# Kernel optimization log

Measured on AMD Instinct MI355X. Metric: run time of the kernel, lower is better.

Reference implementation:

```python
import jax, jax.numpy as jnp
import numpy as np

B, C, H, W = 4, 256, 64, 64
IC = C // 2  # inter_channels default = in_channels // 2


def setup_inputs() -> dict:
    key = jax.random.key(0)
    ks = jax.random.split(key, 7)
    x = jax.random.normal(ks[0], (B, C, H, W), dtype=jnp.float32)
    s = 0.02
    Wq = jax.random.normal(ks[1], (IC, C), dtype=jnp.float32) * s
    bq = jnp.zeros((IC,), dtype=jnp.float32)
    Wk = jax.random.normal(ks[2], (IC, C), dtype=jnp.float32) * s
    bk = jnp.zeros((IC,), dtype=jnp.float32)
    Wv = jax.random.normal(ks[3], (C, C), dtype=jnp.float32) * s
    bv = jnp.zeros((C,), dtype=jnp.float32)
    gamma = jnp.full((1,), 0.1, dtype=jnp.float32)  # nn.Parameter; init 0 in torch, 0.1 here for nontrivial grads
    return {"x": x, "Wq": Wq, "bq": bq, "Wk": Wk, "bk": bk, "Wv": Wv, "bv": bv, "gamma": gamma}


def reference(x, Wq, bq, Wk, bk, Wv, bv, gamma):
    b, c, h, w = x.shape
    n = h * w
    # 1x1 conv projections == per-pixel linear layers
    q = jnp.einsum('bchw,oc->bohw', x, Wq) + bq[None, :, None, None]  # [B,IC,H,W]
    k = jnp.einsum('bchw,oc->bohw', x, Wk) + bk[None, :, None, None]
    v = jnp.einsum('bchw,oc->bohw', x, Wv) + bv[None, :, None, None]  # [B,C,H,W]
    q = q.reshape(b, IC, n).transpose(0, 2, 1)  # [B,N,IC]
    k = k.reshape(b, IC, n)                     # [B,IC,N]
    v = v.reshape(b, c, n)                      # [B,C,N]
    scale = jnp.asarray(IC, x.dtype) ** -0.5
    energy = jnp.einsum('bni,bim->bnm', q, k) * scale  # [B,N,N]
    attn = jax.nn.softmax(energy, axis=-1)             # dropout is identity in eval
    # torch: out = bmm(value, attention.transpose(-1,-2)) -> out[b,c,i] = sum_j v[b,c,j]*attn[b,i,j]
    out = jnp.einsum('bcj,bij->bci', v, attn).reshape(b, c, h, w)
    return gamma[0] * out + 2.0 * x
```

## Files before the change

kernel.cpp:

```cpp
#include <hip/hip_runtime.h>
#include <stdint.h>


#define Bn 4
#define Cn 256
#define ICn 128
#define Nn 4096

typedef __attribute__((ext_vector_type(8))) short bf16x8;
typedef __attribute__((ext_vector_type(4))) float f32x4;
typedef __attribute__((ext_vector_type(16))) float f32x16;

__device__ __forceinline__ unsigned short f2bf(float f) {
  union { float f; uint32_t u; } v; v.f = f;
  uint32_t r = (v.u + 0x7fffu + ((v.u >> 16) & 1u)) >> 16;
  return (unsigned short)r;
}

__device__ __forceinline__ uint32_t pk4_fp8(float a, float b, float c, float d) {
  int r = 0;
  r = __builtin_amdgcn_cvt_pk_fp8_f32(a, b, r, false);
  r = __builtin_amdgcn_cvt_pk_fp8_f32(c, d, r, true);
  return (uint32_t)r;
}

__device__ __forceinline__ void glds16(const uint8_t* g, uint8_t* l) {
  __builtin_amdgcn_global_load_lds((const __attribute__((address_space(1))) void*)g,
                                   (__attribute__((address_space(3))) void*)l, 16, 0, 0);
}

__global__ __launch_bounds__(256) void cvt_weights(const float* __restrict__ Wq,
                                                   const float* __restrict__ Wk,
                                                   const float* __restrict__ Wv,
                                                   unsigned short* __restrict__ wbf) {
  int t = blockIdx.x * 256 + threadIdx.x;
  int tile = t >> 9;
  int kk = (t >> 6) & 7;
  int lane = t & 63;
  const float* W; int row;
  if (tile < 8)       { W = Wq; row = tile * 16 + (lane & 15); }
  else if (tile < 16) { W = Wk; row = (tile - 8) * 16 + (lane & 15); }
  else                { W = Wv; row = (tile - 16) * 16 + (lane & 15); }
  const float* src = W + (size_t)row * Cn + kk * 32 + (lane >> 4) * 8;
  float4 f0 = *(const float4*)src;
  float4 f1 = *(const float4*)(src + 4);
  ushort4 o0, o1;
  o0.x = f2bf(f0.x); o0.y = f2bf(f0.y); o0.z = f2bf(f0.z); o0.w = f2bf(f0.w);
  o1.x = f2bf(f1.x); o1.y = f2bf(f1.y); o1.z = f2bf(f1.z); o1.w = f2bf(f1.w);
  *(ushort4*)(wbf + (size_t)t * 8)     = o0;
  *(ushort4*)(wbf + (size_t)t * 8 + 4) = o1;
}

__global__ __launch_bounds__(256, 2) void proj_kernel(const float* __restrict__ x,
                                                      const unsigned short* __restrict__ wbf,
                                                      const float* __restrict__ bq,
                                                      const float* __restrict__ bk,
                                                      const float* __restrict__ bv,
                                                      uint8_t* __restrict__ qF,
                                                      uint8_t* __restrict__ kF,
                                                      uint8_t* __restrict__ vF) {
  const int b = blockIdx.y;
  const int ntile = blockIdx.x;
  const int px0 = ntile * 32;
  const int tid = threadIdx.x;
  const int lane = tid & 63;
  const int w = tid >> 6;
  const int c0 = lane & 15, g = lane >> 4;
  const float hscale = 0.2973017787506803f;

  __shared__ __align__(16) unsigned short xT[32][264];

  #pragma unroll
  for (int t = 0; t < 8; ++t) {
    int c = (tid >> 3) + t * 32;
    int i8 = tid & 7;
    float4 f4 = *(const float4*)(x + ((size_t)(b * Cn + c)) * Nn + px0 + i8 * 4);
    xT[i8 * 4 + 0][c] = f2bf(f4.x);
    xT[i8 * 4 + 1][c] = f2bf(f4.y);
    xT[i8 * 4 + 2][c] = f2bf(f4.z);
    xT[i8 * 4 + 3][c] = f2bf(f4.w);
  }
  __syncthreads();

  bf16x8 a[2][8];
  #pragma unroll
  for (int h = 0; h < 2; ++h)
    #pragma unroll
    for (int kk = 0; kk < 8; ++kk)
      a[h][kk] = *(const bf16x8*)&xT[h * 16 + c0][kk * 32 + g * 8];

  f32x4 zero = {0.f, 0.f, 0.f, 0.f};

  if (w < 2) {
    const int isq = (w == 0);
    const float* bias = isq ? bq : bk;
    uint8_t* dst = isq ? qF : kF;
    #pragma unroll
    for (int otl = 0; otl < 8; ++otl) {
      const int wt = (isq ? 0 : 8) + otl;
      bf16x8 wf[8];
      #pragma unroll
      for (int kk = 0; kk < 8; ++kk)
        wf[kk] = *(const bf16x8*)(wbf + (((size_t)wt * 8 + kk) << 9) + lane * 8);
      float4 bz = *(const float4*)(bias + otl * 16 + g * 4);
      #pragma unroll
      for (int h = 0; h < 2; ++h) {
        f32x4 acc = zero;
        #pragma unroll
        for (int kk = 0; kk < 8; ++kk)
          acc = __builtin_amdgcn_mfma_f32_16x16x32_bf16(wf[kk], a[h][kk], acc, 0, 0, 0);
        uint32_t d = pk4_fp8((acc[0] + bz.x) * hscale, (acc[1] + bz.y) * hscale,
                             (acc[2] + bz.z) * hscale, (acc[3] + bz.w) * hscale);
        size_t idx = (((((size_t)b * 128 + ntile) * 4 + (otl >> 1)) * 2 + (g >> 1)) * 32
                      + (h * 16 + c0)) * 16 + (otl & 1) * 8 + (g & 1) * 4;
        *(uint32_t*)(dst + idx) = d;
      }
    }
  } else {
    #pragma unroll
    for (int oi = 0; oi < 8; ++oi) {
      const int vtg = (w - 2) * 8 + oi;
      bf16x8 wf[8];
      #pragma unroll
      for (int kk = 0; kk < 8; ++kk)
        wf[kk] = *(const bf16x8*)(wbf + (((size_t)(16 + vtg) * 8 + kk) << 9) + lane * 8);
      const float bias = bv[vtg * 16 + c0];
      #pragma unroll
      for (int h = 0; h < 2; ++h) {
        f32x4 acc = zero;
        #pragma unroll
        for (int kk = 0; kk < 8; ++kk)
          acc = __builtin_amdgcn_mfma_f32_16x16x32_bf16(a[h][kk], wf[kk], acc, 0, 0, 0);
        uint32_t d = pk4_fp8(acc[0] + bias, acc[1] + bias, acc[2] + bias, acc[3] + bias);
        size_t idx = ((((size_t)b * 128 + ntile) * 8 + (vtg >> 1)) * 64
                      + (g >> 1) * 32 + (vtg & 1) * 16 + c0) * 16 + h * 8 + (g & 1) * 4;
        *(uint32_t*)(vF + idx) = d;
      }
    }
  }
}

__global__ __launch_bounds__(256, 2) void attn_kernel(const uint8_t* __restrict__ qF,
                                                      const uint8_t* __restrict__ kF,
                                                      const uint8_t* __restrict__ vF,
                                                      const float* __restrict__ x,
                                                      const float* __restrict__ gamma,
                                                      float* __restrict__ out) {
  const int blk = blockIdx.x;
  const int b = (blk & 7) >> 1;
  const int rg = (blk >> 3) | ((blk & 1) << 6);
  const int n0 = rg * 32;
  const int tid = threadIdx.x;
  const int L = tid & 63;
  const int ks = tid >> 6;
  const int l31 = L & 31, l5 = L >> 5;
  const bool lo = (l5 == 0);

  __shared__ __align__(16) union SM {
    uint8_t vst[4][2][8192];
    struct { float obuf[256][33]; float lsum[4][32]; } e;
  } sm;

  long qf[8];
  {
    const uint8_t* qp = qF + ((size_t)(b * 128 + rg) << 12) + L * 16;
    #pragma unroll
    for (int t = 0; t < 4; ++t) {
      union { uint4 u4; struct { uint64_t lo, hi; } s; } u;
      u.u4 = *(const uint4*)(qp + t * 1024);
      qf[2 * t] = (long)u.s.lo; qf[2 * t + 1] = (long)u.s.hi;
    }
  }

  f32x16 oacc[8];
  #pragma unroll
  for (int ct = 0; ct < 8; ++ct)
    #pragma unroll
    for (int i = 0; i < 16; ++i) oacc[ct][i] = 0.f;
  float lacc = 0.f;

  const uint8_t* kBase = kF + (((size_t)b * 128) << 12) + L * 16;
  const uint8_t* vBaseG = vF + (((size_t)b * 128) << 13);
  uint8_t* vst_w = &sm.vst[tid >> 6][0][0];

  {
    const uint8_t* vp = vBaseG + (((size_t)(ks * 32)) << 13) + (size_t)L * 16;
    #pragma unroll
    for (int ct = 0; ct < 8; ++ct)
      glds16(vp + ct * 1024, vst_w + ct * 1024);
  }
  long kfr[8];
  {
    const uint8_t* kp = kBase + (((size_t)(ks * 32)) << 12);
    #pragma unroll
    for (int t = 0; t < 4; ++t) {
      union { uint4 u4; struct { uint64_t lo, hi; } s; } u;
      u.u4 = *(const uint4*)(kp + t * 1024);
      kfr[2 * t] = (long)u.s.lo; kfr[2 * t + 1] = (long)u.s.hi;
    }
  }

  for (int it = 0; it < 32; ++it) {
    const int cur = it & 1;
    const int kb = ks * 32 + it;

    uint4 vfr[8];
    {
      const uint8_t* vl = vst_w + cur * 8192 + L * 16;
      #pragma unroll
      for (int ct = 0; ct < 8; ++ct) vfr[ct] = *(const uint4*)(vl + ct * 1024);
    }

    f32x16 s;
    #pragma unroll
    for (int i = 0; i < 16; ++i) s[i] = 0.f;
    #pragma unroll
    for (int f = 0; f < 8; ++f)
      s = __builtin_amdgcn_mfma_f32_32x32x16_fp8_fp8(kfr[f], qf[f], s, 0, 0, 0);

    if (it < 31) {
      const uint8_t* vp = vBaseG + (((size_t)(kb + 1)) << 13) + (size_t)L * 16;
      uint8_t* ldst = vst_w + (cur ^ 1) * 8192;
      #pragma unroll
      for (int ct = 0; ct < 8; ++ct)
        glds16(vp + ct * 1024, ldst + ct * 1024);
      const uint8_t* kp = kBase + (((size_t)(kb + 1)) << 12);
      #pragma unroll
      for (int t = 0; t < 4; ++t) {
        union { uint4 u4; struct { uint64_t lo, hi; } s; } u;
        u.u4 = *(const uint4*)(kp + t * 1024);
        kfr[2 * t] = (long)u.s.lo; kfr[2 * t + 1] = (long)u.s.hi;
      }
    }

    float p[16];
    #pragma unroll
    for (int i = 0; i < 16; ++i) p[i] = __expf(s[i]);
    #pragma unroll
    for (int i = 0; i < 16; ++i) lacc += p[i];
    uint32_t d0 = pk4_fp8(p[0], p[1], p[2], p[3]);
    uint32_t d1 = pk4_fp8(p[4], p[5], p[6], p[7]);
    uint32_t d2 = pk4_fp8(p[8], p[9], p[10], p[11]);
    uint32_t d3 = pk4_fp8(p[12], p[13], p[14], p[15]);

    uint32_t X1 = __shfl_xor(lo ? d1 : d0, 32, 64);
    uint32_t X2 = __shfl_xor(lo ? d3 : d2, 32, 64);
    long f0 = lo ? (long)(((uint64_t)X1 << 32) | d0) : (long)(((uint64_t)d1 << 32) | X1);
    long f1 = lo ? (long)(((uint64_t)X2 << 32) | d2) : (long)(((uint64_t)d3 << 32) | X2);

    #pragma unroll
    for (int ct = 0; ct < 8; ++ct) {
      union { uint4 u4; struct { uint64_t lo, hi; } s; } u;
      u.u4 = vfr[ct];
      oacc[ct] = __builtin_amdgcn_mfma_f32_32x32x16_fp8_fp8((long)u.s.lo, f0, oacc[ct], 0, 0, 0);
      oacc[ct] = __builtin_amdgcn_mfma_f32_32x32x16_fp8_fp8((long)u.s.hi, f1, oacc[ct], 0, 0, 0);
    }
  }

  float lfin = lacc + __shfl_xor(lacc, 32, 64);

  #pragma unroll
  for (int pq = 0; pq < 4; ++pq) {
    __syncthreads();
    if (pq == 0 && lo) sm.e.lsum[ks][l31] = lfin;
    if (ks == pq) {
      #pragma unroll
      for (int ct = 0; ct < 8; ++ct) {
        #pragma unroll
        for (int i = 0; i < 16; ++i) {
          int ch = ct * 32 + (i & 3) + 8 * (i >> 2) + 4 * l5;
          if (pq == 0) sm.e.obuf[ch][l31] = oacc[ct][i];
          else         sm.e.obuf[ch][l31] += oacc[ct][i];
        }
      }
    }
  }
  __syncthreads();

  const int row = tid & 31;
  const float coef = gamma[0] / (sm.e.lsum[0][row] + sm.e.lsum[1][row] +
                                 sm.e.lsum[2][row] + sm.e.lsum[3][row]);
  #pragma unroll 4
  for (int t = 0; t < 32; ++t) {
    int ch = (tid >> 5) + t * 8;
    size_t off = ((size_t)(b * Cn + ch)) * Nn + n0 + row;
    out[off] = sm.e.obuf[ch][row] * coef + 2.0f * x[off];
  }
}

extern "C" void kernel_launch(void* const* d_in, const int* in_sizes, int n_in,
                              void* d_out, int out_size, void* d_ws, size_t ws_size,
                              hipStream_t stream) {
  const float* x     = (const float*)d_in[0];
  const float* Wq    = (const float*)d_in[1];
  const float* bq    = (const float*)d_in[2];
  const float* Wk    = (const float*)d_in[3];
  const float* bk    = (const float*)d_in[4];
  const float* Wv    = (const float*)d_in[5];
  const float* bv    = (const float*)d_in[6];
  const float* gamma = (const float*)d_in[7];
  float* out = (float*)d_out;

  uint8_t* qF = (uint8_t*)d_ws;
  uint8_t* kF = qF + (2u << 20);
  uint8_t* vF = kF + (2u << 20);
  unsigned short* wbf = (unsigned short*)(vF + (4u << 20));

  hipLaunchKernelGGL(cvt_weights, dim3(64), dim3(256), 0, stream, Wq, Wk, Wv, wbf);
  hipLaunchKernelGGL(proj_kernel, dim3(128, 4), dim3(256), 0, stream,
                     x, wbf, bq, bk, bv, qF, kF, vF);
  hipLaunchKernelGGL(attn_kernel, dim3(512), dim3(256), 0, stream,
                     qF, kF, vF, x, gamma, out);
}
```

Before: 141.0 us.

## Deepen attention prefetch to two stages with manual waitcnt, setprio, and exp2 scaling

Restructures the attention main loop into a templated, two-at-a-time unrolled iteration. Each step prefetches the K/V tiles two blocks ahead into a ping-pong buffer and waits on explicit vmcnt/lgkmcnt counts, so global-load latency is better hidden behind the MFMA work. MFMA sections are wrapped in s_setprio to favour matrix issue across waves. The log2(e) factor is folded into the Q/K projection scale so the softmax can call raw v_exp_f32 instead of __expf, saving a multiply per element. In exchange the kernel holds two K register sets, which raises register pressure, and its correctness now depends on hand-set wait counts.

```diff
diff --git a/kernel.cpp b/kernel.cpp
--- a/kernel.cpp
+++ b/kernel.cpp
@@ -66,7 +66,7 @@
   const int lane = tid & 63;
   const int w = tid >> 6;
   const int c0 = lane & 15, g = lane >> 4;
-  const float hscale = 0.2973017787506803f;
+  const float hscale = 0.3570958292f;
 
   __shared__ __align__(16) unsigned short xT[32][264];
 
@@ -138,6 +138,78 @@
       }
     }
   }
+}
+
+template <int CUR, bool PRE, int WAITN>
+__device__ __forceinline__ void attn_iter(int it, int ks, int L, bool lo,
+                                          const uint8_t* kBase, const uint8_t* vBaseG,
+                                          uint8_t* vst_w, long (&qf)[8],
+                                          long (&kfr0)[8], long (&kfr1)[8],
+                                          f32x16 (&oacc)[8], float& lacc) {
+  long (&kfr)[8] = CUR ? kfr1 : kfr0;
+
+  asm volatile("s_waitcnt vmcnt(%0)" :: "n"(WAITN) : "memory");
+  __builtin_amdgcn_sched_barrier(0);
+
+  uint4 vfr[8];
+  {
+    const uint8_t* vl = vst_w + CUR * 8192 + (size_t)L * 16;
+    #pragma unroll
+    for (int ct = 0; ct < 8; ++ct) vfr[ct] = *(const uint4*)(vl + ct * 1024);
+  }
+
+  f32x16 s;
+  #pragma unroll
+  for (int i = 0; i < 16; ++i) s[i] = 0.f;
+  __builtin_amdgcn_s_setprio(1);
+  #pragma unroll
+  for (int f = 0; f < 8; ++f)
+    s = __builtin_amdgcn_mfma_f32_32x32x16_fp8_fp8(kfr[f], qf[f], s, 0, 0, 0);
+  __builtin_amdgcn_s_setprio(0);
+
+  float p[16];
+  #pragma unroll
+  for (int i = 0; i < 16; ++i)
+    asm("v_exp_f32 %0, %1" : "=v"(p[i]) : "v"(s[i]));
+  #pragma unroll
+  for (int i = 0; i < 16; ++i) lacc += p[i];
+  uint32_t d0 = pk4_fp8(p[0], p[1], p[2], p[3]);
+  uint32_t d1 = pk4_fp8(p[4], p[5], p[6], p[7]);
+  uint32_t d2 = pk4_fp8(p[8], p[9], p[10], p[11]);
+  uint32_t d3 = pk4_fp8(p[12], p[13], p[14], p[15]);
+
+  uint32_t X1 = __shfl_xor(lo ? d1 : d0, 32, 64);
+  uint32_t X2 = __shfl_xor(lo ? d3 : d2, 32, 64);
+  long f0 = lo ? (long)(((uint64_t)X1 << 32) | d0) : (long)(((uint64_t)d1 << 32) | X1);
+  long f1 = lo ? (long)(((uint64_t)X2 << 32) | d2) : (long)(((uint64_t)d3 << 32) | X2);
+
+  if (PRE) {
+    asm volatile("s_waitcnt lgkmcnt(0)" ::: "memory");
+    __builtin_amdgcn_sched_barrier(0);
+    const int kt = ks * 32 + it + 2;
+    const uint8_t* vp = vBaseG + ((size_t)kt << 13) + (size_t)L * 16;
+    uint8_t* ldst = vst_w + CUR * 8192;
+    #pragma unroll
+    for (int ct = 0; ct < 8; ++ct)
+      glds16(vp + ct * 1024, ldst + ct * 1024);
+    const uint8_t* kp = kBase + ((size_t)kt << 12);
+    #pragma unroll
+    for (int t = 0; t < 4; ++t) {
+      union { uint4 u4; struct { uint64_t lo2, hi2; } s2; } u;
+      u.u4 = *(const uint4*)(kp + t * 1024);
+      kfr[2 * t] = (long)u.s2.lo2; kfr[2 * t + 1] = (long)u.s2.hi2;
+    }
+  }
+
+  __builtin_amdgcn_s_setprio(1);
+  #pragma unroll
+  for (int ct = 0; ct < 8; ++ct) {
+    union { uint4 u4; struct { uint64_t lo2, hi2; } s2; } u;
+    u.u4 = vfr[ct];
+    oacc[ct] = __builtin_amdgcn_mfma_f32_32x32x16_fp8_fp8((long)u.s2.lo2, f0, oacc[ct], 0, 0, 0);
+    oacc[ct] = __builtin_amdgcn_mfma_f32_32x32x16_fp8_fp8((long)u.s2.hi2, f1, oacc[ct], 0, 0, 0);
+  }
+  __builtin_amdgcn_s_setprio(0);
 }
 
 __global__ __launch_bounds__(256, 2) void attn_kernel(const uint8_t* __restrict__ qF,
@@ -183,79 +255,45 @@
   const uint8_t* vBaseG = vF + (((size_t)b * 128) << 13);
   uint8_t* vst_w = &sm.vst[tid >> 6][0][0];
 
-  {
-    const uint8_t* vp = vBaseG + (((size_t)(ks * 32)) << 13) + (size_t)L * 16;
+  long kfr0[8], kfr1[8];
+
+  {
+    const uint8_t* vp = vBaseG + (((size_t)(ks * 32 + 0)) << 13) + (size_t)L * 16;
     #pragma unroll
     for (int ct = 0; ct < 8; ++ct)
-      glds16(vp + ct * 1024, vst_w + ct * 1024);
-  }
-  long kfr[8];
-  {
-    const uint8_t* kp = kBase + (((size_t)(ks * 32)) << 12);
+      glds16(vp + ct * 1024, vst_w + 0 * 8192 + ct * 1024);
+  }
+  {
+    const uint8_t* kp = kBase + (((size_t)(ks * 32 + 0)) << 12);
     #pragma unroll
     for (int t = 0; t < 4; ++t) {
-      union { uint4 u4; struct { uint64_t lo, hi; } s; } u;
+      union { uint4 u4; struct { uint64_t lo2, hi2; } s2; } u;
       u.u4 = *(const uint4*)(kp + t * 1024);
-      kfr[2 * t] = (long)u.s.lo; kfr[2 * t + 1] = (long)u.s.hi;
-    }
-  }
-
-  for (int it = 0; it < 32; ++it) {
-    const int cur = it & 1;
-    const int kb = ks * 32 + it;
-
-    uint4 vfr[8];
-    {
-      const uint8_t* vl = vst_w + cur * 8192 + L * 16;
-      #pragma unroll
-      for (int ct = 0; ct < 8; ++ct) vfr[ct] = *(const uint4*)(vl + ct * 1024);
-    }
-
-    f32x16 s;
-    #pragma unroll
-    for (int i = 0; i < 16; ++i) s[i] = 0.f;
-    #pragma unroll
-    for (int f = 0; f < 8; ++f)
-      s = __builtin_amdgcn_mfma_f32_32x32x16_fp8_fp8(kfr[f], qf[f], s, 0, 0, 0);
-
-    if (it < 31) {
-      const uint8_t* vp = vBaseG + (((size_t)(kb + 1)) << 13) + (size_t)L * 16;
-      uint8_t* ldst = vst_w + (cur ^ 1) * 8192;
-      #pragma unroll
-      for (int ct = 0; ct < 8; ++ct)
-        glds16(vp + ct * 1024, ldst + ct * 1024);
-      const uint8_t* kp = kBase + (((size_t)(kb + 1)) << 12);
-      #pragma unroll
-      for (int t = 0; t < 4; ++t) {
-        union { uint4 u4; struct { uint64_t lo, hi; } s; } u;
-        u.u4 = *(const uint4*)(kp + t * 1024);
-        kfr[2 * t] = (long)u.s.lo; kfr[2 * t + 1] = (long)u.s.hi;
-      }
-    }
-
-    float p[16];
-    #pragma unroll
-    for (int i = 0; i < 16; ++i) p[i] = __expf(s[i]);
-    #pragma unroll
-    for (int i = 0; i < 16; ++i) lacc += p[i];
-    uint32_t d0 = pk4_fp8(p[0], p[1], p[2], p[3]);
-    uint32_t d1 = pk4_fp8(p[4], p[5], p[6], p[7]);
-    uint32_t d2 = pk4_fp8(p[8], p[9], p[10], p[11]);
-    uint32_t d3 = pk4_fp8(p[12], p[13], p[14], p[15]);
-
-    uint32_t X1 = __shfl_xor(lo ? d1 : d0, 32, 64);
-    uint32_t X2 = __shfl_xor(lo ? d3 : d2, 32, 64);
-    long f0 = lo ? (long)(((uint64_t)X1 << 32) | d0) : (long)(((uint64_t)d1 << 32) | X1);
-    long f1 = lo ? (long)(((uint64_t)X2 << 32) | d2) : (long)(((uint64_t)d3 << 32) | X2);
-
-    #pragma unroll
-    for (int ct = 0; ct < 8; ++ct) {
-      union { uint4 u4; struct { uint64_t lo, hi; } s; } u;
-      u.u4 = vfr[ct];
-      oacc[ct] = __builtin_amdgcn_mfma_f32_32x32x16_fp8_fp8((long)u.s.lo, f0, oacc[ct], 0, 0, 0);
-      oacc[ct] = __builtin_amdgcn_mfma_f32_32x32x16_fp8_fp8((long)u.s.hi, f1, oacc[ct], 0, 0, 0);
-    }
-  }
+      kfr0[2 * t] = (long)u.s2.lo2; kfr0[2 * t + 1] = (long)u.s2.hi2;
+    }
+  }
+  {
+    const uint8_t* vp = vBaseG + (((size_t)(ks * 32 + 1)) << 13) + (size_t)L * 16;
+    #pragma unroll
+    for (int ct = 0; ct < 8; ++ct)
+      glds16(vp + ct * 1024, vst_w + 1 * 8192 + ct * 1024);
+  }
+  {
+    const uint8_t* kp = kBase + (((size_t)(ks * 32 + 1)) << 12);
+    #pragma unroll
+    for (int t = 0; t < 4; ++t) {
+      union { uint4 u4; struct { uint64_t lo2, hi2; } s2; } u;
+      u.u4 = *(const uint4*)(kp + t * 1024);
+      kfr1[2 * t] = (long)u.s2.lo2; kfr1[2 * t + 1] = (long)u.s2.hi2;
+    }
+  }
+
+  for (int i2 = 0; i2 < 15; ++i2) {
+    attn_iter<0, true, 12>(2 * i2,     ks, L, lo, kBase, vBaseG, vst_w, qf, kfr0, kfr1, oacc, lacc);
+    attn_iter<1, true, 12>(2 * i2 + 1, ks, L, lo, kBase, vBaseG, vst_w, qf, kfr0, kfr1, oacc, lacc);
+  }
+  attn_iter<0, false, 12>(30, ks, L, lo, kBase, vBaseG, vst_w, qf, kfr0, kfr1, oacc, lacc);
+  attn_iter<1, false, 0>(31, ks, L, lo, kBase, vBaseG, vst_w, qf, kfr0, kfr1, oacc, lacc);
 
   float lfin = lacc + __shfl_xor(lacc, 32, 64);
 
```

Result: slower. 152.0 us (+7.8%).

## Software-pipeline attention QK^T one tile ahead with double-buffered K and permlane swap

Applied to the files above, without the earlier changes.

Restructures the attention loop so the score MFMA for the next key tile is issued while the current tile's exponentials and PV MFMAs run, with K fragments double-buffered two tiles ahead. It replaces __expf with raw v_exp_f32, which computes 2^x, and compensates by folding log2(e) into the projection scale constant. It also replaces the shuffle and select sequence with v_permlane32_swap. The aim is to hide MFMA and load latency behind the transcendental work, at the cost of more registers for a second score accumulator and a second K buffer.

```diff
diff --git a/kernel.cpp b/kernel.cpp
--- a/kernel.cpp
+++ b/kernel.cpp
@@ -66,7 +66,7 @@
   const int lane = tid & 63;
   const int w = tid >> 6;
   const int c0 = lane & 15, g = lane >> 4;
-  const float hscale = 0.2973017787506803f;
+  const float hscale = 0.3570958292f;
 
   __shared__ __align__(16) unsigned short xT[32][264];
 
@@ -137,6 +137,76 @@
         *(uint32_t*)(vF + idx) = d;
       }
     }
+  }
+}
+
+template <int P, bool PREK, bool LAST>
+__device__ __forceinline__ void attn_body(int t, int ks, int L,
+                                          const uint8_t* kBase, const uint8_t* vBaseG,
+                                          uint8_t* vst_w, const long (&qf)[8],
+                                          long (&kfr0)[8], long (&kfr1)[8],
+                                          f32x16& s_cur, f32x16& s_next,
+                                          f32x16 (&oacc)[8], float& lacc) {
+  uint4 vfr[8];
+  {
+    const uint8_t* vl = vst_w + P * 8192 + (size_t)L * 16;
+    #pragma unroll
+    for (int ct = 0; ct < 8; ++ct) vfr[ct] = *(const uint4*)(vl + ct * 1024);
+  }
+
+  if constexpr (!LAST) {
+    const uint8_t* vp = vBaseG + (((size_t)(ks * 32 + t + 1)) << 13) + (size_t)L * 16;
+    uint8_t* ldst = vst_w + (P ^ 1) * 8192;
+    #pragma unroll
+    for (int ct = 0; ct < 8; ++ct)
+      glds16(vp + ct * 1024, ldst + ct * 1024);
+  }
+  if constexpr (PREK) {
+    long (&kfrP)[8] = P ? kfr1 : kfr0;
+    const uint8_t* kp = kBase + (((size_t)(ks * 32 + t + 2)) << 12);
+    #pragma unroll
+    for (int q = 0; q < 4; ++q) {
+      union { uint4 u4; struct { uint64_t lo2, hi2; } s2; } u;
+      u.u4 = *(const uint4*)(kp + q * 1024);
+      kfrP[2 * q] = (long)u.s2.lo2; kfrP[2 * q + 1] = (long)u.s2.hi2;
+    }
+  }
+
+  #pragma unroll
+  for (int i = 0; i < 16; ++i) {
+    float r;
+    asm("v_exp_f32 %0, %1" : "=v"(r) : "v"(s_cur[i]));
+    s_cur[i] = r;
+  }
+
+  if constexpr (!LAST) {
+    long (&kn)[8] = P ? kfr0 : kfr1;
+    #pragma unroll
+    for (int i = 0; i < 16; ++i) s_next[i] = 0.f;
+    #pragma unroll
+    for (int f = 0; f < 8; ++f)
+      s_next = __builtin_amdgcn_mfma_f32_32x32x16_fp8_fp8(kn[f], qf[f], s_next, 0, 0, 0);
+  }
+
+  #pragma unroll
+  for (int i = 0; i < 16; ++i) lacc += s_cur[i];
+  uint32_t d0 = pk4_fp8(s_cur[0], s_cur[1], s_cur[2], s_cur[3]);
+  uint32_t d1 = pk4_fp8(s_cur[4], s_cur[5], s_cur[6], s_cur[7]);
+  uint32_t d2 = pk4_fp8(s_cur[8], s_cur[9], s_cur[10], s_cur[11]);
+  uint32_t d3 = pk4_fp8(s_cur[12], s_cur[13], s_cur[14], s_cur[15]);
+  uint32_t a0 = d1, b0 = d0;
+  asm("v_permlane32_swap_b32 %0, %1" : "+v"(a0), "+v"(b0));
+  long f0 = (long)(((uint64_t)a0 << 32) | b0);
+  uint32_t a1 = d3, b1 = d2;
+  asm("v_permlane32_swap_b32 %0, %1" : "+v"(a1), "+v"(b1));
+  long f1 = (long)(((uint64_t)a1 << 32) | b1);
+
+  #pragma unroll
+  for (int ct = 0; ct < 8; ++ct) {
+    union { uint4 u4; struct { uint64_t lo2, hi2; } s2; } u;
+    u.u4 = vfr[ct];
+    oacc[ct] = __builtin_amdgcn_mfma_f32_32x32x16_fp8_fp8((long)u.s2.lo2, f0, oacc[ct], 0, 0, 0);
+    oacc[ct] = __builtin_amdgcn_mfma_f32_32x32x16_fp8_fp8((long)u.s2.hi2, f1, oacc[ct], 0, 0, 0);
   }
 }
 
@@ -154,7 +224,6 @@
   const int L = tid & 63;
   const int ks = tid >> 6;
   const int l31 = L & 31, l5 = L >> 5;
-  const bool lo = (l5 == 0);
 
   __shared__ __align__(16) union SM {
     uint8_t vst[4][2][8192];
@@ -183,81 +252,48 @@
   const uint8_t* vBaseG = vF + (((size_t)b * 128) << 13);
   uint8_t* vst_w = &sm.vst[tid >> 6][0][0];
 
+  long kfr0[8], kfr1[8];
+  f32x16 s_a, s_b;
+
   {
     const uint8_t* vp = vBaseG + (((size_t)(ks * 32)) << 13) + (size_t)L * 16;
     #pragma unroll
     for (int ct = 0; ct < 8; ++ct)
       glds16(vp + ct * 1024, vst_w + ct * 1024);
   }
-  long kfr[8];
   {
     const uint8_t* kp = kBase + (((size_t)(ks * 32)) << 12);
     #pragma unroll
-    for (int t = 0; t < 4; ++t) {
-      union { uint4 u4; struct { uint64_t lo, hi; } s; } u;
-      u.u4 = *(const uint4*)(kp + t * 1024);
-      kfr[2 * t] = (long)u.s.lo; kfr[2 * t + 1] = (long)u.s.hi;
-    }
-  }
-
-  for (int it = 0; it < 32; ++it) {
-    const int cur = it & 1;
-    const int kb = ks * 32 + it;
-
-    uint4 vfr[8];
-    {
-      const uint8_t* vl = vst_w + cur * 8192 + L * 16;
-      #pragma unroll
-      for (int ct = 0; ct < 8; ++ct) vfr[ct] = *(const uint4*)(vl + ct * 1024);
-    }
-
-    f32x16 s;
-    #pragma unroll
-    for (int i = 0; i < 16; ++i) s[i] = 0.f;
-    #pragma unroll
-    for (int f = 0; f < 8; ++f)
-      s = __builtin_amdgcn_mfma_f32_32x32x16_fp8_fp8(kfr[f], qf[f], s, 0, 0, 0);
-
-    if (it < 31) {
-      const uint8_t* vp = vBaseG + (((size_t)(kb + 1)) << 13) + (size_t)L * 16;
-      uint8_t* ldst = vst_w + (cur ^ 1) * 8192;
-      #pragma unroll
-      for (int ct = 0; ct < 8; ++ct)
-        glds16(vp + ct * 1024, ldst + ct * 1024);
-      const uint8_t* kp = kBase + (((size_t)(kb + 1)) << 12);
-      #pragma unroll
-      for (int t = 0; t < 4; ++t) {
-        union { uint4 u4; struct { uint64_t lo, hi; } s; } u;
-        u.u4 = *(const uint4*)(kp + t * 1024);
-        kfr[2 * t] = (long)u.s.lo; kfr[2 * t + 1] = (long)u.s.hi;
-      }
-    }
-
-    float p[16];
-    #pragma unroll
-    for (int i = 0; i < 16; ++i) p[i] = __expf(s[i]);
-    #pragma unroll
-    for (int i = 0; i < 16; ++i) lacc += p[i];
-    uint32_t d0 = pk4_fp8(p[0], p[1], p[2], p[3]);
-    uint32_t d1 = pk4_fp8(p[4], p[5], p[6], p[7]);
-    uint32_t d2 = pk4_fp8(p[8], p[9], p[10], p[11]);
-    uint32_t d3 = pk4_fp8(p[12], p[13], p[14], p[15]);
-
-    uint32_t X1 = __shfl_xor(lo ? d1 : d0, 32, 64);
-    uint32_t X2 = __shfl_xor(lo ? d3 : d2, 32, 64);
-    long f0 = lo ? (long)(((uint64_t)X1 << 32) | d0) : (long)(((uint64_t)d1 << 32) | X1);
-    long f1 = lo ? (long)(((uint64_t)X2 << 32) | d2) : (long)(((uint64_t)d3 << 32) | X2);
-
-    #pragma unroll
-    for (int ct = 0; ct < 8; ++ct) {
-      union { uint4 u4; struct { uint64_t lo, hi; } s; } u;
-      u.u4 = vfr[ct];
-      oacc[ct] = __builtin_amdgcn_mfma_f32_32x32x16_fp8_fp8((long)u.s.lo, f0, oacc[ct], 0, 0, 0);
-      oacc[ct] = __builtin_amdgcn_mfma_f32_32x32x16_fp8_fp8((long)u.s.hi, f1, oacc[ct], 0, 0, 0);
-    }
-  }
+    for (int q = 0; q < 4; ++q) {
+      union { uint4 u4; struct { uint64_t lo2, hi2; } s2; } u;
+      u.u4 = *(const uint4*)(kp + q * 1024);
+      kfr0[2 * q] = (long)u.s2.lo2; kfr0[2 * q + 1] = (long)u.s2.hi2;
+    }
+  }
+  {
+    const uint8_t* kp = kBase + (((size_t)(ks * 32 + 1)) << 12);
+    #pragma unroll
+    for (int q = 0; q < 4; ++q) {
+      union { uint4 u4; struct { uint64_t lo2, hi2; } s2; } u;
+      u.u4 = *(const uint4*)(kp + q * 1024);
+      kfr1[2 * q] = (long)u.s2.lo2; kfr1[2 * q + 1] = (long)u.s2.hi2;
+    }
+  }
+  #pragma unroll
+  for (int i = 0; i < 16; ++i) s_a[i] = 0.f;
+  #pragma unroll
+  for (int f = 0; f < 8; ++f)
+    s_a = __builtin_amdgcn_mfma_f32_32x32x16_fp8_fp8(kfr0[f], qf[f], s_a, 0, 0, 0);
+
+  for (int i2 = 0; i2 < 15; ++i2) {
+    attn_body<0, true, false>(2 * i2,     ks, L, kBase, vBaseG, vst_w, qf, kfr0, kfr1, s_a, s_b, oacc, lacc);
+    attn_body<1, true, false>(2 * i2 + 1, ks, L, kBase, vBaseG, vst_w, qf, kfr0, kfr1, s_b, s_a, oacc, lacc);
+  }
+  attn_body<0, false, false>(30, ks, L, kBase, vBaseG, vst_w, qf, kfr0, kfr1, s_a, s_b, oacc, lacc);
+  attn_body<1, false, true>(31, ks, L, kBase, vBaseG, vst_w, qf, kfr0, kfr1, s_b, s_a, oacc, lacc);
 
   float lfin = lacc + __shfl_xor(lacc, 32, 64);
+  const bool lo = (l5 == 0);
 
   #pragma unroll
   for (int pq = 0; pq < 4; ++pq) {
```

New measurement: 147.6 us. 1.05x slower.
